# Kernel optimization log

Measured on AMD Instinct MI355X. Metric: run time of the kernel, lower is better.

Reference implementation:

```python
import jax, jax.numpy as jnp
import numpy as np

B, S, D = 4, 2048, 1024
NEG_INF = jnp.float32(-jnp.inf)


def setup_inputs() -> dict:
    key = jax.random.key(0)
    kx, kq, kk, kv = jax.random.split(key, 4)
    scale = 0.02
    return {
        "x": jax.random.normal(kx, (B, S, D), dtype=jnp.float32),
        "Wq": jax.random.normal(kq, (D, D), dtype=jnp.float32) * scale,
        "Wk": jax.random.normal(kk, (D, D), dtype=jnp.float32) * scale,
        "Wv": jax.random.normal(kv, (D, D), dtype=jnp.float32) * scale,
    }


def reference(x, Wq, Wk, Wv):
    # nn.Linear(d_in, d_out): y = x @ W.T (no bias; qkv_bias=False)
    q = jnp.einsum("bsd,ed->bse", x, Wq)
    k = jnp.einsum("bsd,ed->bse", x, Wk)
    v = jnp.einsum("bsd,ed->bse", x, Wv)
    n = x.shape[1]
    scores = jnp.einsum("bqe,bke->bqk", q, k)  # [B, S, S]
    # causal mask: positions k > q are masked with -inf
    causal = jnp.tril(jnp.ones((n, n), dtype=bool))
    scores = jnp.where(causal[None, :, :], scores, NEG_INF)
    attn = jax.nn.softmax(scores / jnp.sqrt(jnp.float32(k.shape[-1])), axis=-1)
    # dropout p=0.0 (eval) -> identity
    return jnp.einsum("bqk,bke->bqe", attn, v)
```

## Files before the change

kernel.cpp:

```cpp
#include <hip/hip_runtime.h>
#include <hip/hip_bf16.h>
#include <stdint.h>
#include <stddef.h>


typedef __hip_bfloat16 bf16;
typedef short short8 __attribute__((ext_vector_type(8)));
typedef short short4v __attribute__((ext_vector_type(4)));
typedef float f32x4 __attribute__((ext_vector_type(4)));

#define BM 128
#define BN 128
#define BK 64
#define MSZ 8192
#define DD 1024

__device__ __forceinline__ void cstore(float* p, float v) { *p = v; }
__device__ __forceinline__ void cstore(bf16* p, float v) { *p = __float2bfloat16(v); }

__global__ __launch_bounds__(256)
void f2b(const float* __restrict__ s, bf16* __restrict__ d, int n) {
  const int i = (blockIdx.x * 256 + threadIdx.x) * 4;
  if (i >= n) return;
  const float4 v = *(const float4*)(s + i);
  bf16 t[4] = {__float2bfloat16(v.x), __float2bfloat16(v.y),
               __float2bfloat16(v.z), __float2bfloat16(v.w)};
  *(short4v*)(d + i) = *(short4v*)t;
}

__global__ __launch_bounds__(256)
void f2b3(const float* __restrict__ a, const float* __restrict__ b,
          const float* __restrict__ c, bf16* __restrict__ d, int n) {
  const float* s = (blockIdx.y == 0) ? a : (blockIdx.y == 1) ? b : c;
  const int i = (blockIdx.x * 256 + threadIdx.x) * 4;
  if (i >= n) return;
  const float4 v = *(const float4*)(s + i);
  bf16 t[4] = {__float2bfloat16(v.x), __float2bfloat16(v.y),
               __float2bfloat16(v.z), __float2bfloat16(v.w)};
  *(short4v*)(d + (size_t)blockIdx.y * n + i) = *(short4v*)t;
}

template <int MODE, typename CT>
__global__ __launch_bounds__(256, 4)
void gemm_bt(const bf16* __restrict__ A, const bf16* __restrict__ B,
             CT* __restrict__ C, bf16* __restrict__ C2,
             int lda, int ldb, int ldc, int K,
             long sA, long sB, long sC, float scale) {
  int by, bx, zb;
  const int flat = blockIdx.x;
  const int c = flat & 7, j = flat >> 3;
  if (MODE == 1) {
    by = c * 8 + (j & 7);
    bx = j >> 3;
    zb = 0;
  } else if (MODE == 2) {
    zb = c >> 1;
    const int t = (c & 1) * 68 + j;
    by = (int)((__fsqrt_rn(8.f * (float)t + 1.f) - 1.f) * 0.5f);
    while ((by + 1) * (by + 2) / 2 <= t) by++;
    while (by * (by + 1) / 2 > t) by--;
    bx = t - by * (by + 1) / 2;
  } else {
    zb = c >> 1;
    bx = j & 7;
    by = 2 * (7 - (j >> 3)) + (c & 1);
  }

  __shared__ short8 As[1024];
  __shared__ short8 Bs[1024];

  const int tid = threadIdx.x;
  const int wave = tid >> 6, lane = tid & 63;
  const int wm = wave >> 1, wn = wave & 1;
  const int l15 = lane & 15, q4 = lane >> 4;
  const int bm0 = by * BM, bn0 = bx * BN;

  const bf16* Az = A + (long)zb * sA;
  const bf16* Bz = B + (long)zb * sB;
  CT* Cz = C + (long)zb * sC;

  const int sg = lane >> 3, sr = lane & 7;
  const bf16* apg = Az + (size_t)(bm0 + wave * 32 + sr) * lda + sg * 8;
  const bf16* bpg = Bz + (size_t)(bn0 + wave * 32 + sr) * ldb + sg * 8;
  short8* asw = &As[wave * 256];
  short8* bsw = &Bs[wave * 256];

  const int Ke = (MODE == 3) ? min(K, (by + 1) * BM) : K;

  const int rh = l15 >> 3, r3 = l15 & 7;
  const int fra = wm * 512 + rh * 64 + q4 * 8 + r3;
  const int frb = wn * 512 + rh * 64 + q4 * 8 + r3;

  f32x4 acc[4][4] = {};

  for (int k0 = 0; k0 < Ke; k0 += BK) {
#pragma unroll
    for (int jj = 0; jj < 4; jj++) {
      __builtin_amdgcn_global_load_lds(apg + (size_t)jj * 8 * lda + k0,
                                       asw + jj * 64, 16, 0, 0);
      __builtin_amdgcn_global_load_lds(bpg + (size_t)jj * 8 * ldb + k0,
                                       bsw + jj * 64, 16, 0, 0);
    }
    __syncthreads();

#pragma unroll
    for (int s = 0; s < 2; s++) {
      short8 af[4], bfr[4];
#pragma unroll
      for (int i = 0; i < 4; i++) af[i] = As[fra + i * 128 + s * 32];
#pragma unroll
      for (int jj = 0; jj < 4; jj++) bfr[jj] = Bs[frb + jj * 128 + s * 32];
#pragma unroll
      for (int i = 0; i < 4; i++)
#pragma unroll
        for (int jj = 0; jj < 4; jj++)
          acc[i][jj] = __builtin_amdgcn_mfma_f32_16x16x32_bf16(af[i], bfr[jj], acc[i][jj], 0, 0, 0);
    }
    __syncthreads();
  }

  if (MODE == 1 && bx >= 16) {
#pragma unroll
    for (int i = 0; i < 4; i++) {
#pragma unroll
      for (int jj = 0; jj < 4; jj++) {
        const int rowb = bm0 + wm * 64 + i * 16 + q4 * 4;
        const int v = (bn0 - 2048) + wn * 64 + jj * 16 + l15;
        bf16 t[4] = {__float2bfloat16(acc[i][jj][0]), __float2bfloat16(acc[i][jj][1]),
                     __float2bfloat16(acc[i][jj][2]), __float2bfloat16(acc[i][jj][3])};
        *(short4v*)(C2 + (size_t)v * MSZ + rowb) = *(short4v*)t;
      }
    }
    return;
  }

  CT* Cb = Cz;
  int coff = bn0;
  if (MODE == 1) {
    Cb = Cz + (bx >= 8 ? (size_t)MSZ * DD : 0);
    coff = (bx & 7) * BN;
  }
#pragma unroll
  for (int i = 0; i < 4; i++) {
#pragma unroll
    for (int jj = 0; jj < 4; jj++) {
#pragma unroll
      for (int r = 0; r < 4; r++) {
        const int row = bm0 + wm * 64 + i * 16 + q4 * 4 + r;
        const int col = coff + wn * 64 + jj * 16 + l15;
        cstore(&Cb[(size_t)row * ldc + col], acc[i][jj][r] * scale);
      }
    }
  }
}

__global__ __launch_bounds__(256)
void softmax_rows(const bf16* __restrict__ Sc, bf16* __restrict__ P, int S) {
  const int q = blockIdx.x, b = blockIdx.y;
  const short8* srow = (const short8*)(Sc + ((size_t)b * S + q) * S);
  short8* prow = (short8*)(P + ((size_t)b * S + q) * S);
  const int len = q + 1;
  const int tid = threadIdx.x;
  const int wave = tid >> 6, lane = tid & 63;
  __shared__ float red[10];

  const short8 raw = srow[tid];
  float v[8];
#pragma unroll
  for (int j = 0; j < 8; j++) {
    const int k = tid * 8 + j;
    const float f = __bfloat162float(((const bf16*)&raw)[j]);
    v[j] = (k < len) ? f : -1e30f;
  }

  float m = v[0];
#pragma unroll
  for (int j = 1; j < 8; j++) m = fmaxf(m, v[j]);
#pragma unroll
  for (int o = 32; o; o >>= 1) m = fmaxf(m, __shfl_down(m, o));
  if (lane == 0) red[wave] = m;
  __syncthreads();
  if (tid == 0) red[8] = fmaxf(fmaxf(red[0], red[1]), fmaxf(red[2], red[3]));
  __syncthreads();
  const float M = red[8];

  float e[8], s = 0.f;
#pragma unroll
  for (int j = 0; j < 8; j++) { e[j] = __expf(v[j] - M); s += e[j]; }
#pragma unroll
  for (int o = 32; o; o >>= 1) s += __shfl_down(s, o);
  if (lane == 0) red[4 + wave] = s;
  __syncthreads();
  if (tid == 0) red[9] = red[4] + red[5] + red[6] + red[7];
  __syncthreads();
  const float inv = 1.f / red[9];

  short8 outp;
#pragma unroll
  for (int j = 0; j < 8; j++) {
    const int k = tid * 8 + j;
    ((bf16*)&outp)[j] = __float2bfloat16((k < len) ? e[j] * inv : 0.f);
  }
  prow[tid] = outp;
}

extern "C" void kernel_launch(void* const* d_in, const int* in_sizes, int n_in,
                              void* d_out, int out_size, void* d_ws, size_t ws_size,
                              hipStream_t stream) {
  const float* x  = (const float*)d_in[0];
  const float* Wq = (const float*)d_in[1];
  const float* Wk = (const float*)d_in[2];
  const float* Wv = (const float*)d_in[3];
  float* out = (float*)d_out;

  const int Bb = 4, S = 2048, D = 1024, MS = Bb * S;

  char* ws = (char*)d_ws;
  bf16* xb = (bf16*)ws;
  bf16* wb = (bf16*)(ws + (size_t)MS * D * 2);
  bf16* Q  = (bf16*)(ws + (size_t)MS * D * 2 + 3u * D * D * 2);
  bf16* Kp = Q + (size_t)MS * D;
  bf16* VT = Kp + (size_t)MS * D;
  bf16* Sc = VT + (size_t)MS * D;
  bf16* P  = (bf16*)ws;
  (void)Kp;

  dim3 blk(256);

  f2b<<<dim3(MS * D / 4 / 256), blk, 0, stream>>>(x, xb, MS * D);
  f2b3<<<dim3(D * D / 4 / 256, 3), blk, 0, stream>>>(Wq, Wk, Wv, wb, D * D);

  gemm_bt<1, bf16><<<dim3(1536), blk, 0, stream>>>(
      xb, wb, Q, VT, D, D, D, D, 0, 0, 0, 1.f);
  gemm_bt<2, bf16><<<dim3(544), blk, 0, stream>>>(
      Q, Kp, Sc, nullptr, D, D, S, D,
      (long)S * D, (long)S * D, (long)S * S, 0.03125f);
  softmax_rows<<<dim3(S, Bb), blk, 0, stream>>>(Sc, P, S);
  gemm_bt<3, float><<<dim3(512), blk, 0, stream>>>(
      P, VT, out, nullptr, S, MS, D, S,
      (long)S * S, (long)S, (long)S * D, 1.f);
}
```

Measured before the change: 307.4 us.

## Double GEMM K-tile to 128 and make projection blocks process two tiles

Raises the GEMM K-step from 64 to 128, doubling LDS tiles to 64 KB total, which halves the number of barrier pairs per K loop. Lowers the occupancy hint from 4 to 2 blocks per CU to match the larger shared memory. The QKV projection GEMM now launches 768 blocks, each looping over two output tiles, to reduce launch and wave-tail overhead. The risk is lower occupancy and less latency hiding, since loads are still not overlapped with compute.

New measurement: 325.2 us. +5.8%, slower.

```diff
diff --git a/kernel.cpp b/kernel.cpp
--- a/kernel.cpp
+++ b/kernel.cpp
@@ -11,7 +11,7 @@
 
 #define BM 128
 #define BN 128
-#define BK 64
+#define BK 128
 #define MSZ 8192
 #define DD 1024
 
@@ -41,114 +41,123 @@
 }
 
 template <int MODE, typename CT>
-__global__ __launch_bounds__(256, 4)
+__global__ __launch_bounds__(256, 2)
 void gemm_bt(const bf16* __restrict__ A, const bf16* __restrict__ B,
              CT* __restrict__ C, bf16* __restrict__ C2,
              int lda, int ldb, int ldc, int K,
              long sA, long sB, long sC, float scale) {
-  int by, bx, zb;
-  const int flat = blockIdx.x;
-  const int c = flat & 7, j = flat >> 3;
-  if (MODE == 1) {
-    by = c * 8 + (j & 7);
-    bx = j >> 3;
-    zb = 0;
-  } else if (MODE == 2) {
-    zb = c >> 1;
-    const int t = (c & 1) * 68 + j;
-    by = (int)((__fsqrt_rn(8.f * (float)t + 1.f) - 1.f) * 0.5f);
-    while ((by + 1) * (by + 2) / 2 <= t) by++;
-    while (by * (by + 1) / 2 > t) by--;
-    bx = t - by * (by + 1) / 2;
-  } else {
-    zb = c >> 1;
-    bx = j & 7;
-    by = 2 * (7 - (j >> 3)) + (c & 1);
-  }
-
-  __shared__ short8 As[1024];
-  __shared__ short8 Bs[1024];
+  __shared__ short8 As[2048];
+  __shared__ short8 Bs[2048];
 
   const int tid = threadIdx.x;
   const int wave = tid >> 6, lane = tid & 63;
   const int wm = wave >> 1, wn = wave & 1;
   const int l15 = lane & 15, q4 = lane >> 4;
-  const int bm0 = by * BM, bn0 = bx * BN;
-
-  const bf16* Az = A + (long)zb * sA;
-  const bf16* Bz = B + (long)zb * sB;
-  CT* Cz = C + (long)zb * sC;
-
+  const int rh = l15 >> 3, r3 = l15 & 7;
   const int sg = lane >> 3, sr = lane & 7;
-  const bf16* apg = Az + (size_t)(bm0 + wave * 32 + sr) * lda + sg * 8;
-  const bf16* bpg = Bz + (size_t)(bn0 + wave * 32 + sr) * ldb + sg * 8;
-  short8* asw = &As[wave * 256];
-  short8* bsw = &Bs[wave * 256];
-
-  const int Ke = (MODE == 3) ? min(K, (by + 1) * BM) : K;
-
-  const int rh = l15 >> 3, r3 = l15 & 7;
-  const int fra = wm * 512 + rh * 64 + q4 * 8 + r3;
-  const int frb = wn * 512 + rh * 64 + q4 * 8 + r3;
-
-  f32x4 acc[4][4] = {};
-
-  for (int k0 = 0; k0 < Ke; k0 += BK) {
-#pragma unroll
-    for (int jj = 0; jj < 4; jj++) {
-      __builtin_amdgcn_global_load_lds(apg + (size_t)jj * 8 * lda + k0,
-                                       asw + jj * 64, 16, 0, 0);
-      __builtin_amdgcn_global_load_lds(bpg + (size_t)jj * 8 * ldb + k0,
-                                       bsw + jj * 64, 16, 0, 0);
+  const int flat = blockIdx.x;
+  const int c = flat & 7;
+
+  const int fra = wm * 1024 + rh * 128 + q4 * 8 + r3;
+  const int frb = wn * 1024 + rh * 128 + q4 * 8 + r3;
+  short8* asw = &As[wave * 512];
+  short8* bsw = &Bs[wave * 512];
+
+  const int NJOBS = (MODE == 1) ? 2 : 1;
+
+  for (int jb = 0; jb < NJOBS; ++jb) {
+    int by, bx, zb;
+    if (MODE == 1) {
+      const int j = (flat >> 3) + jb * 96;
+      by = c * 8 + (j & 7);
+      bx = j >> 3;
+      zb = 0;
+    } else if (MODE == 2) {
+      zb = c >> 1;
+      const int t = (c & 1) * 68 + (flat >> 3);
+      int y = (int)((__fsqrt_rn(8.f * (float)t + 1.f) - 1.f) * 0.5f);
+      while ((y + 1) * (y + 2) / 2 <= t) y++;
+      while (y * (y + 1) / 2 > t) y--;
+      by = y;
+      bx = t - y * (y + 1) / 2;
+    } else {
+      const int j = flat >> 3;
+      zb = c >> 1;
+      bx = j & 7;
+      by = 2 * (7 - (j >> 3)) + (c & 1);
     }
-    __syncthreads();
-
-#pragma unroll
-    for (int s = 0; s < 2; s++) {
-      short8 af[4], bfr[4];
-#pragma unroll
-      for (int i = 0; i < 4; i++) af[i] = As[fra + i * 128 + s * 32];
-#pragma unroll
-      for (int jj = 0; jj < 4; jj++) bfr[jj] = Bs[frb + jj * 128 + s * 32];
-#pragma unroll
-      for (int i = 0; i < 4; i++)
-#pragma unroll
-        for (int jj = 0; jj < 4; jj++)
-          acc[i][jj] = __builtin_amdgcn_mfma_f32_16x16x32_bf16(af[i], bfr[jj], acc[i][jj], 0, 0, 0);
+
+    const int bm0 = by * BM, bn0 = bx * BN;
+    const bf16* Az = A + (long)zb * sA;
+    const bf16* Bz = B + (long)zb * sB;
+    CT* Cz = C + (long)zb * sC;
+
+    const bf16* apg = Az + (size_t)(bm0 + wave * 32 + sr) * lda + sg * 8;
+    const bf16* bpg = Bz + (size_t)(bn0 + wave * 32 + sr) * ldb + sg * 8;
+
+    const int Ke = (MODE == 3) ? min(K, (by + 1) * BM) : K;
+
+    f32x4 acc[4][4] = {};
+
+    for (int k0 = 0; k0 < Ke; k0 += BK) {
+#pragma unroll
+      for (int jj = 0; jj < 4; jj++) {
+#pragma unroll
+        for (int h = 0; h < 2; h++) {
+          __builtin_amdgcn_global_load_lds(apg + (size_t)jj * 8 * lda + h * 64 + k0,
+                                           asw + jj * 128 + h * 64, 16, 0, 0);
+          __builtin_amdgcn_global_load_lds(bpg + (size_t)jj * 8 * ldb + h * 64 + k0,
+                                           bsw + jj * 128 + h * 64, 16, 0, 0);
+        }
+      }
+      __syncthreads();
+
+#pragma unroll
+      for (int s = 0; s < 4; s++) {
+        short8 af[4], bfr[4];
+#pragma unroll
+        for (int i = 0; i < 4; i++) af[i] = As[fra + i * 256 + s * 32];
+#pragma unroll
+        for (int jj = 0; jj < 4; jj++) bfr[jj] = Bs[frb + jj * 256 + s * 32];
+#pragma unroll
+        for (int i = 0; i < 4; i++)
+#pragma unroll
+          for (int jj = 0; jj < 4; jj++)
+            acc[i][jj] = __builtin_amdgcn_mfma_f32_16x16x32_bf16(af[i], bfr[jj], acc[i][jj], 0, 0, 0);
+      }
+      __syncthreads();
     }
-    __syncthreads();
-  }
-
-  if (MODE == 1 && bx >= 16) {
-#pragma unroll
-    for (int i = 0; i < 4; i++) {
-#pragma unroll
-      for (int jj = 0; jj < 4; jj++) {
-        const int rowb = bm0 + wm * 64 + i * 16 + q4 * 4;
-        const int v = (bn0 - 2048) + wn * 64 + jj * 16 + l15;
-        bf16 t[4] = {__float2bfloat16(acc[i][jj][0]), __float2bfloat16(acc[i][jj][1]),
-                     __float2bfloat16(acc[i][jj][2]), __float2bfloat16(acc[i][jj][3])};
-        *(short4v*)(C2 + (size_t)v * MSZ + rowb) = *(short4v*)t;
-      }
-    }
-    return;
-  }
-
-  CT* Cb = Cz;
-  int coff = bn0;
-  if (MODE == 1) {
-    Cb = Cz + (bx >= 8 ? (size_t)MSZ * DD : 0);
-    coff = (bx & 7) * BN;
-  }
-#pragma unroll
-  for (int i = 0; i < 4; i++) {
-#pragma unroll
-    for (int jj = 0; jj < 4; jj++) {
-#pragma unroll
-      for (int r = 0; r < 4; r++) {
-        const int row = bm0 + wm * 64 + i * 16 + q4 * 4 + r;
-        const int col = coff + wn * 64 + jj * 16 + l15;
-        cstore(&Cb[(size_t)row * ldc + col], acc[i][jj][r] * scale);
+
+    if (MODE == 1 && bx >= 16) {
+#pragma unroll
+      for (int i = 0; i < 4; i++) {
+#pragma unroll
+        for (int jj = 0; jj < 4; jj++) {
+          const int rowb = bm0 + wm * 64 + i * 16 + q4 * 4;
+          const int v = (bn0 - 2048) + wn * 64 + jj * 16 + l15;
+          bf16 t[4] = {__float2bfloat16(acc[i][jj][0]), __float2bfloat16(acc[i][jj][1]),
+                       __float2bfloat16(acc[i][jj][2]), __float2bfloat16(acc[i][jj][3])};
+          *(short4v*)(C2 + (size_t)v * MSZ + rowb) = *(short4v*)t;
+        }
+      }
+    } else {
+      CT* Cb = Cz;
+      int coff = bn0;
+      if (MODE == 1) {
+        Cb = Cz + (bx >= 8 ? (size_t)MSZ * DD : 0);
+        coff = (bx & 7) * BN;
+      }
+#pragma unroll
+      for (int i = 0; i < 4; i++) {
+#pragma unroll
+        for (int jj = 0; jj < 4; jj++) {
+#pragma unroll
+          for (int r = 0; r < 4; r++) {
+            const int row = bm0 + wm * 64 + i * 16 + q4 * 4 + r;
+            const int col = coff + wn * 64 + jj * 16 + l15;
+            cstore(&Cb[(size_t)row * ldc + col], acc[i][jj][r] * scale);
+          }
+        }
       }
     }
   }
@@ -230,7 +239,7 @@
   f2b<<<dim3(MS * D / 4 / 256), blk, 0, stream>>>(x, xb, MS * D);
   f2b3<<<dim3(D * D / 4 / 256, 3), blk, 0, stream>>>(Wq, Wk, Wv, wb, D * D);
 
-  gemm_bt<1, bf16><<<dim3(1536), blk, 0, stream>>>(
+  gemm_bt<1, bf16><<<dim3(768), blk, 0, stream>>>(
       xb, wb, Q, VT, D, D, D, D, 0, 0, 0, 1.f);
   gemm_bt<2, bf16><<<dim3(544), blk, 0, stream>>>(
       Q, Kp, Sc, nullptr, D, D, S, D,
```

## Fuse softmax exponentiation and normalization into the PV GEMM

Applied to the files above, without the earlier changes.

The softmax kernel no longer writes a normalized probability matrix. It now computes only the per-row max and inverse sum into a small stats buffer. The PV GEMM reads raw scores directly from global memory into registers, exponentiates them against the row max, and scales the outputs by the inverse sum in its epilogue. The QK GEMM writes -1e30 into masked diagonal-tile entries so the fused path stays causal. This removes one full write and read of the SxS probability matrix, but the A operand now bypasses LDS staging, uses uncoalesced direct loads, and recomputes exp once per column tile.

After: 351.1 us. +14.2%, slower.

```diff
diff --git a/kernel.cpp b/kernel.cpp
--- a/kernel.cpp
+++ b/kernel.cpp
@@ -78,6 +78,7 @@
   const bf16* Az = A + (long)zb * sA;
   const bf16* Bz = B + (long)zb * sB;
   CT* Cz = C + (long)zb * sC;
+  const float2* mz = (const float2*)C2;
 
   const int sg = lane >> 3, sr = lane & 7;
   const bf16* apg = Az + (size_t)(bm0 + wave * 32 + sr) * lda + sg * 8;
@@ -91,23 +92,56 @@
   const int fra = wm * 512 + rh * 64 + q4 * 8 + r3;
   const int frb = wn * 512 + rh * 64 + q4 * 8 + r3;
 
+  const bf16* adir = Az + (size_t)(bm0 + wm * 64 + l15) * lda + q4 * 8;
+  float Mi[4];
+  if (MODE == 3) {
+#pragma unroll
+    for (int i = 0; i < 4; i++)
+      Mi[i] = mz[(size_t)zb * 2048 + bm0 + wm * 64 + i * 16 + l15].x;
+  }
+
   f32x4 acc[4][4] = {};
 
   for (int k0 = 0; k0 < Ke; k0 += BK) {
-#pragma unroll
-    for (int jj = 0; jj < 4; jj++) {
-      __builtin_amdgcn_global_load_lds(apg + (size_t)jj * 8 * lda + k0,
-                                       asw + jj * 64, 16, 0, 0);
+    if (MODE != 3) {
+#pragma unroll
+      for (int jj = 0; jj < 4; jj++)
+        __builtin_amdgcn_global_load_lds(apg + (size_t)jj * 8 * lda + k0,
+                                         asw + jj * 64, 16, 0, 0);
+    }
+#pragma unroll
+    for (int jj = 0; jj < 4; jj++)
       __builtin_amdgcn_global_load_lds(bpg + (size_t)jj * 8 * ldb + k0,
                                        bsw + jj * 64, 16, 0, 0);
+
+    short8 ar0[4], ar1[4];
+    if (MODE == 3) {
+#pragma unroll
+      for (int i = 0; i < 4; i++)
+        ar0[i] = *(const short8*)(adir + (size_t)(i * 16) * lda + k0);
+#pragma unroll
+      for (int i = 0; i < 4; i++)
+        ar1[i] = *(const short8*)(adir + (size_t)(i * 16) * lda + k0 + 32);
     }
     __syncthreads();
 
 #pragma unroll
     for (int s = 0; s < 2; s++) {
       short8 af[4], bfr[4];
-#pragma unroll
-      for (int i = 0; i < 4; i++) af[i] = As[fra + i * 128 + s * 32];
+      if (MODE == 3) {
+#pragma unroll
+        for (int i = 0; i < 4; i++) {
+          const short8 raw = (s == 0) ? ar0[i] : ar1[i];
+#pragma unroll
+          for (int e = 0; e < 8; e++) {
+            const float f = __bfloat162float(((const bf16*)&raw)[e]);
+            ((bf16*)&af[i])[e] = __float2bfloat16(__expf(f - Mi[i]));
+          }
+        }
+      } else {
+#pragma unroll
+        for (int i = 0; i < 4; i++) af[i] = As[fra + i * 128 + s * 32];
+      }
 #pragma unroll
       for (int jj = 0; jj < 4; jj++) bfr[jj] = Bs[frb + jj * 128 + s * 32];
 #pragma unroll
@@ -134,6 +168,15 @@
     return;
   }
 
+  float iz[4][4];
+  if (MODE == 3) {
+#pragma unroll
+    for (int i = 0; i < 4; i++)
+#pragma unroll
+      for (int r = 0; r < 4; r++)
+        iz[i][r] = mz[(size_t)zb * 2048 + bm0 + wm * 64 + i * 16 + q4 * 4 + r].y;
+  }
+
   CT* Cb = Cz;
   int coff = bn0;
   if (MODE == 1) {
@@ -148,17 +191,19 @@
       for (int r = 0; r < 4; r++) {
         const int row = bm0 + wm * 64 + i * 16 + q4 * 4 + r;
         const int col = coff + wn * 64 + jj * 16 + l15;
-        cstore(&Cb[(size_t)row * ldc + col], acc[i][jj][r] * scale);
+        float vv = acc[i][jj][r] * scale;
+        if (MODE == 2 && by == bx && col > row) vv = -1e30f;
+        if (MODE == 3) vv = acc[i][jj][r] * iz[i][r];
+        cstore(&Cb[(size_t)row * ldc + col], vv);
       }
     }
   }
 }
 
 __global__ __launch_bounds__(256)
-void softmax_rows(const bf16* __restrict__ Sc, bf16* __restrict__ P, int S) {
+void row_stats(const bf16* __restrict__ Sc, float2* __restrict__ mz, int S) {
   const int q = blockIdx.x, b = blockIdx.y;
   const short8* srow = (const short8*)(Sc + ((size_t)b * S + q) * S);
-  short8* prow = (short8*)(P + ((size_t)b * S + q) * S);
   const int len = q + 1;
   const int tid = threadIdx.x;
   const int wave = tid >> 6, lane = tid & 63;
@@ -184,24 +229,17 @@
   __syncthreads();
   const float M = red[8];
 
-  float e[8], s = 0.f;
-#pragma unroll
-  for (int j = 0; j < 8; j++) { e[j] = __expf(v[j] - M); s += e[j]; }
+  float s = 0.f;
+#pragma unroll
+  for (int j = 0; j < 8; j++) s += __expf(v[j] - M);
 #pragma unroll
   for (int o = 32; o; o >>= 1) s += __shfl_down(s, o);
   if (lane == 0) red[4 + wave] = s;
   __syncthreads();
-  if (tid == 0) red[9] = red[4] + red[5] + red[6] + red[7];
-  __syncthreads();
-  const float inv = 1.f / red[9];
-
-  short8 outp;
-#pragma unroll
-  for (int j = 0; j < 8; j++) {
-    const int k = tid * 8 + j;
-    ((bf16*)&outp)[j] = __float2bfloat16((k < len) ? e[j] * inv : 0.f);
-  }
-  prow[tid] = outp;
+  if (tid == 0) {
+    const float Z = red[4] + red[5] + red[6] + red[7];
+    mz[(size_t)b * S + q] = make_float2(M, 1.f / Z);
+  }
 }
 
 extern "C" void kernel_launch(void* const* d_in, const int* in_sizes, int n_in,
@@ -222,7 +260,7 @@
   bf16* Kp = Q + (size_t)MS * D;
   bf16* VT = Kp + (size_t)MS * D;
   bf16* Sc = VT + (size_t)MS * D;
-  bf16* P  = (bf16*)ws;
+  float2* mz = (float2*)(Sc + (size_t)Bb * S * S);
   (void)Kp;
 
   dim3 blk(256);
@@ -235,8 +273,8 @@
   gemm_bt<2, bf16><<<dim3(544), blk, 0, stream>>>(
       Q, Kp, Sc, nullptr, D, D, S, D,
       (long)S * D, (long)S * D, (long)S * S, 0.03125f);
-  softmax_rows<<<dim3(S, Bb), blk, 0, stream>>>(Sc, P, S);
+  row_stats<<<dim3(S, Bb), blk, 0, stream>>>(Sc, mz, S);
   gemm_bt<3, float><<<dim3(512), blk, 0, stream>>>(
-      P, VT, out, nullptr, S, MS, D, S,
+      Sc, VT, out, (bf16*)mz, S, MS, D, S,
       (long)S * S, (long)S, (long)S * D, 1.f);
 }
```

## Replace QKV projection GEMM with double-buffered 256x128 tile, 8-wave kernel

Applied to the files above, without the earlier changes.

Adds a dedicated QKV projection kernel using 512 threads, 256x128 output tiles and double-buffered LDS. It prefetches the next K-slice with direct global-to-LDS loads while MFMAs run on the current buffer, using explicit vmcnt waits, barriers and setprio around the MFMA block. The goal is to hide global load latency and improve operand reuse in the largest GEMM. In exchange it uses more LDS per block and allows only one block per CU, so overlap depends on the 8 waves within each block.

Result: faster. 292.3 us (-4.9%).

```diff
diff --git a/kernel.cpp b/kernel.cpp
--- a/kernel.cpp
+++ b/kernel.cpp
@@ -40,6 +40,105 @@
   *(short4v*)(d + (size_t)blockIdx.y * n + i) = *(short4v*)t;
 }
 
+__global__ __launch_bounds__(512, 1)
+void qkv_8p(const bf16* __restrict__ A, const bf16* __restrict__ B,
+            bf16* __restrict__ C, bf16* __restrict__ C2) {
+  __shared__ short8 As[2][2048];
+  __shared__ short8 Bs[2][1024];
+
+  const int flat = blockIdx.x;
+  const int c = flat & 7, j = flat >> 3;
+  const int by = c * 4 + (j & 3), bx = j >> 2;
+  const int bm0 = by * 256, bn0 = bx * 128;
+  const int tid = threadIdx.x, wave = tid >> 6, lane = tid & 63;
+  const int wm = wave >> 1, wn = wave & 1;
+  const int l15 = lane & 15, q4 = lane >> 4;
+  const int rh = l15 >> 3, r3 = l15 & 7;
+  const int sr = lane & 7, sgk = (lane >> 3) & 3, shb = lane >> 5;
+
+  const bf16* apg = A + (size_t)(bm0 + wave * 32 + shb * 8 + sr) * DD + sgk * 8;
+  const bf16* bpg = B + (size_t)(bn0 + wave * 16 + shb * 8 + sr) * DD + sgk * 8;
+
+  const int NT = DD / 64;
+
+  auto stage = [&](int t, int ks) {
+    const int b = t & 1;
+    const size_t ko = (size_t)(t * 64 + ks * 32);
+#pragma unroll
+    for (int i = 0; i < 2; i++)
+      __builtin_amdgcn_global_load_lds(apg + (size_t)(i * 16) * DD + ko,
+                                       &As[b][ks * 1024 + wave * 128 + i * 64], 16, 0, 0);
+    __builtin_amdgcn_global_load_lds(bpg + ko,
+                                     &Bs[b][ks * 512 + wave * 64], 16, 0, 0);
+  };
+
+  const int fa = wm * 256 + rh * 32 + q4 * 8 + r3;
+  const int fb = wn * 256 + rh * 32 + q4 * 8 + r3;
+
+  f32x4 acc[4][4] = {};
+
+  stage(0, 0);
+  stage(0, 1);
+  asm volatile("s_waitcnt vmcnt(3)" ::: "memory");
+  asm volatile("s_barrier" ::: "memory");
+
+  for (int t = 0; t < NT; ++t) {
+    const int b = t & 1;
+#pragma unroll
+    for (int ks = 0; ks < 2; ++ks) {
+      short8 af[4], bfr[4];
+#pragma unroll
+      for (int i = 0; i < 4; i++) af[i] = As[b][ks * 1024 + fa + i * 64];
+#pragma unroll
+      for (int jj = 0; jj < 4; jj++) bfr[jj] = Bs[b][ks * 512 + fb + jj * 64];
+      if (t + 1 < NT) {
+        stage(t + 1, ks);
+        asm volatile("s_waitcnt vmcnt(3)" ::: "memory");
+      } else {
+        asm volatile("s_waitcnt vmcnt(0)" ::: "memory");
+      }
+      asm volatile("s_barrier" ::: "memory");
+      __builtin_amdgcn_s_setprio(1);
+#pragma unroll
+      for (int i = 0; i < 4; i++)
+#pragma unroll
+        for (int jj = 0; jj < 4; jj++)
+          acc[i][jj] = __builtin_amdgcn_mfma_f32_16x16x32_bf16(af[i], bfr[jj], acc[i][jj], 0, 0, 0);
+      __builtin_amdgcn_s_setprio(0);
+      asm volatile("s_barrier" ::: "memory");
+    }
+  }
+
+  if (bx >= 16) {
+#pragma unroll
+    for (int i = 0; i < 4; i++) {
+#pragma unroll
+      for (int jj = 0; jj < 4; jj++) {
+        const int rowb = bm0 + wm * 64 + i * 16 + q4 * 4;
+        const int v = (bn0 - 2048) + wn * 64 + jj * 16 + l15;
+        bf16 t4[4] = {__float2bfloat16(acc[i][jj][0]), __float2bfloat16(acc[i][jj][1]),
+                      __float2bfloat16(acc[i][jj][2]), __float2bfloat16(acc[i][jj][3])};
+        *(short4v*)(C2 + (size_t)v * MSZ + rowb) = *(short4v*)t4;
+      }
+    }
+    return;
+  }
+  bf16* Cb = C + (bx >= 8 ? (size_t)MSZ * DD : 0);
+  const int coff = (bx & 7) * 128;
+#pragma unroll
+  for (int i = 0; i < 4; i++) {
+#pragma unroll
+    for (int jj = 0; jj < 4; jj++) {
+#pragma unroll
+      for (int r = 0; r < 4; r++) {
+        const int row = bm0 + wm * 64 + i * 16 + q4 * 4 + r;
+        const int col = coff + wn * 64 + jj * 16 + l15;
+        Cb[(size_t)row * DD + col] = __float2bfloat16(acc[i][jj][r]);
+      }
+    }
+  }
+}
+
 template <int MODE, typename CT>
 __global__ __launch_bounds__(256, 4)
 void gemm_bt(const bf16* __restrict__ A, const bf16* __restrict__ B,
@@ -49,11 +148,7 @@
   int by, bx, zb;
   const int flat = blockIdx.x;
   const int c = flat & 7, j = flat >> 3;
-  if (MODE == 1) {
-    by = c * 8 + (j & 7);
-    bx = j >> 3;
-    zb = 0;
-  } else if (MODE == 2) {
+  if (MODE == 2) {
     zb = c >> 1;
     const int t = (c & 1) * 68 + j;
     by = (int)((__fsqrt_rn(8.f * (float)t + 1.f) - 1.f) * 0.5f);
@@ -119,27 +214,6 @@
     __syncthreads();
   }
 
-  if (MODE == 1 && bx >= 16) {
-#pragma unroll
-    for (int i = 0; i < 4; i++) {
-#pragma unroll
-      for (int jj = 0; jj < 4; jj++) {
-        const int rowb = bm0 + wm * 64 + i * 16 + q4 * 4;
-        const int v = (bn0 - 2048) + wn * 64 + jj * 16 + l15;
-        bf16 t[4] = {__float2bfloat16(acc[i][jj][0]), __float2bfloat16(acc[i][jj][1]),
-                     __float2bfloat16(acc[i][jj][2]), __float2bfloat16(acc[i][jj][3])};
-        *(short4v*)(C2 + (size_t)v * MSZ + rowb) = *(short4v*)t;
-      }
-    }
-    return;
-  }
-
-  CT* Cb = Cz;
-  int coff = bn0;
-  if (MODE == 1) {
-    Cb = Cz + (bx >= 8 ? (size_t)MSZ * DD : 0);
-    coff = (bx & 7) * BN;
-  }
 #pragma unroll
   for (int i = 0; i < 4; i++) {
 #pragma unroll
@@ -147,8 +221,8 @@
 #pragma unroll
       for (int r = 0; r < 4; r++) {
         const int row = bm0 + wm * 64 + i * 16 + q4 * 4 + r;
-        const int col = coff + wn * 64 + jj * 16 + l15;
-        cstore(&Cb[(size_t)row * ldc + col], acc[i][jj][r] * scale);
+        const int col = bn0 + wn * 64 + jj * 16 + l15;
+        cstore(&Cz[(size_t)row * ldc + col], acc[i][jj][r] * scale);
       }
     }
   }
@@ -230,8 +304,7 @@
   f2b<<<dim3(MS * D / 4 / 256), blk, 0, stream>>>(x, xb, MS * D);
   f2b3<<<dim3(D * D / 4 / 256, 3), blk, 0, stream>>>(Wq, Wk, Wv, wb, D * D);
 
-  gemm_bt<1, bf16><<<dim3(1536), blk, 0, stream>>>(
-      xb, wb, Q, VT, D, D, D, D, 0, 0, 0, 1.f);
+  qkv_8p<<<dim3(768), dim3(512), 0, stream>>>(xb, wb, Q, VT);
   gemm_bt<2, bf16><<<dim3(544), blk, 0, stream>>>(
       Q, Kp, Sc, nullptr, D, D, S, D,
       (long)S * D, (long)S * D, (long)S * S, 0.03125f);
```
